# Performance work log

Measured on AMD Instinct MI355X. Metric: run time of the kernel, lower is better.

Reference implementation:

```python
import jax, jax.numpy as jnp
import numpy as np

C = 1024
H = 16
D = C // H  # head_dim = 64
FF = 4 * C


def setup_inputs() -> dict:
    key = jax.random.key(0)
    ks = jax.random.split(key, 10)
    s = lambda fan_in: 1.0 / np.sqrt(fan_in)
    return {
        "x": jax.random.normal(ks[0], (2, 2048, C), dtype=jnp.float32),
        "ln1_g": jnp.ones((C,), jnp.float32),
        "ln1_b": jnp.zeros((C,), jnp.float32),
        "w_qkv": jax.random.normal(ks[1], (C, 3 * C), jnp.float32) * s(C),
        "w_proj": jax.random.normal(ks[2], (C, C), jnp.float32) * s(C),
        "b_proj": jnp.zeros((C,), jnp.float32),
        "ln2_g": jnp.ones((C,), jnp.float32),
        "ln2_b": jnp.zeros((C,), jnp.float32),
        "w_fc1": jax.random.normal(ks[3], (C, FF), jnp.float32) * s(C),
        "b_fc1": jnp.zeros((FF,), jnp.float32),
        "w_fc2": jax.random.normal(ks[4], (FF, C), jnp.float32) * s(FF),
        "b_fc2": jnp.zeros((C,), jnp.float32),
    }


def _layernorm(x, g, b, eps=1e-5):
    mu = jnp.mean(x, axis=-1, keepdims=True)
    var = jnp.var(x, axis=-1, keepdims=True)
    return (x - mu) * jax.lax.rsqrt(var + eps) * g + b


def reference(x, ln1_g, ln1_b, w_qkv, w_proj, b_proj, ln2_g, ln2_b, w_fc1, b_fc1, w_fc2, b_fc2):
    B, N, _ = x.shape
    scale = D ** -0.5
    # --- attention sub-block (pre-LN) ---
    h = _layernorm(x, ln1_g, ln1_b)
    qkv = (h @ w_qkv).reshape(B, N, 3, H, D)
    q, k, v = jnp.moveaxis(qkv, 2, 0)          # each [B, N, H, D]
    attn = jnp.einsum("bnhd,bmhd->bhnm", q, k) * scale  # [B,H,N,N]
    attn = jax.nn.softmax(attn, axis=-1)
    o = jnp.einsum("bhnm,bmhd->bnhd", attn, v).reshape(B, N, C)
    x = x + o @ w_proj + b_proj
    # --- MLP sub-block (pre-LN) ---
    h = _layernorm(x, ln2_g, ln2_b)
    h = jax.nn.gelu(h @ w_fc1 + b_fc1, approximate=False)
    x = x + h @ w_fc2 + b_fc2
    return x
```

## Files before the change

### kernel.cpp

```cpp
#include <hip/hip_runtime.h>
#include <hip/hip_bf16.h>

typedef unsigned short u16;
typedef unsigned int u32;
typedef __attribute__((ext_vector_type(8))) short bf16x8;
typedef __attribute__((ext_vector_type(4))) float f32x4;
typedef __attribute__((ext_vector_type(4))) int   i32x4;
typedef __attribute__((ext_vector_type(4))) float fvec4;
typedef __attribute__((ext_vector_type(4))) unsigned int u32x4;

__device__ inline u16 f2bf(float f) {
    union { float f; unsigned u; } v; v.f = f;
    unsigned r = v.u + 0x7fffu + ((v.u >> 16) & 1u);
    return (u16)(r >> 16);
}

__device__ inline u32 cvtpk(float lo, float hi) {
    u32 r;
    asm("v_cvt_pk_bf16_f32 %0, %1, %2" : "=v"(r) : "v"(lo), "v"(hi));
    return r;
}

__device__ inline f32x4 mfma16(bf16x8 a, bf16x8 b, f32x4 c) {
    return __builtin_amdgcn_mfma_f32_16x16x32_bf16(a, b, c, 0, 0, 0);
}

__device__ inline void gload16(const void* g, void* l) {
    __builtin_amdgcn_global_load_lds(
        (const __attribute__((address_space(1))) unsigned int*)g,
        (__attribute__((address_space(3))) unsigned int*)l, 16, 0, 0);
}

__global__ __launch_bounds__(256)
void transpose_all(const float* __restrict__ w0, u16* __restrict__ o0,
                   const float* __restrict__ w1, u16* __restrict__ o1,
                   const float* __restrict__ w2, u16* __restrict__ o2,
                   const float* __restrict__ w3, u16* __restrict__ o3) {
    __shared__ float tile[32][33];
    int b = blockIdx.x;
    const float* in; u16* out; int K, N, local;
    if (b < 3072)      { in = w0; out = o0; K = 1024; N = 3072; local = b; }
    else if (b < 4096) { in = w1; out = o1; K = 1024; N = 1024; local = b - 3072; }
    else if (b < 8192) { in = w2; out = o2; K = 1024; N = 4096; local = b - 4096; }
    else               { in = w3; out = o3; K = 4096; N = 1024; local = b - 8192; }
    const int nx = N >> 5;
    const int n0 = (local % nx) * 32, k0 = (local / nx) * 32;
    const int x = threadIdx.x & 31, y = threadIdx.x >> 5;
    for (int i = 0; i < 4; ++i)
        tile[y + i * 8][x] = in[(size_t)(k0 + y + i * 8) * N + n0 + x];
    __syncthreads();
    for (int i = 0; i < 4; ++i) {
        int r = y + i * 8;
        out[(size_t)(n0 + r) * K + k0 + x] = f2bf(tile[x][r]);
    }
}

__global__ __launch_bounds__(256)
void vtrans(const u16* __restrict__ qkv, u16* __restrict__ vT) {
    __shared__ u32 tl[64][33];
    const int t0 = blockIdx.x * 64, f0 = blockIdx.y * 64;
    const int a = threadIdx.x & 31, yy = threadIdx.x >> 5;
    for (int i = 0; i < 8; ++i) {
        int t = yy + i * 8;
        tl[t][a] = *(const u32*)(qkv + (size_t)(t0 + t) * 3072 + 2048 + f0 + a * 2);
    }
    __syncthreads();
    for (int i = 0; i < 8; ++i) {
        int f = yy + i * 8;
        u32 lo = tl[2 * a][f >> 1], hi = tl[2 * a + 1][f >> 1];
        u32 r = (f & 1) ? ((lo >> 16) | (hi & 0xffff0000u))
                        : ((lo & 0xffffu) | (hi << 16));
        *(u32*)(vT + (size_t)(f0 + f) * 4096 + t0 + 2 * a) = r;
    }
}

__global__ __launch_bounds__(256)
void ln_kernel(const float* __restrict__ x, const float* __restrict__ g,
               const float* __restrict__ bvec, u16* __restrict__ out) {
    __shared__ float red[2][4];
    const int row = blockIdx.x, tid = threadIdx.x;
    const float* xr = x + (size_t)row * 1024;
    fvec4 v = *(const fvec4*)(xr + tid * 4);
    float s  = v[0] + v[1] + v[2] + v[3];
    float s2 = v[0]*v[0] + v[1]*v[1] + v[2]*v[2] + v[3]*v[3];
    for (int off = 1; off < 64; off <<= 1) {
        s  += __shfl_xor(s,  off);
        s2 += __shfl_xor(s2, off);
    }
    const int w = tid >> 6;
    if ((tid & 63) == 0) { red[0][w] = s; red[1][w] = s2; }
    __syncthreads();
    s  = red[0][0] + red[0][1] + red[0][2] + red[0][3];
    s2 = red[1][0] + red[1][1] + red[1][2] + red[1][3];
    const float mu  = s * (1.0f / 1024.0f);
    const float var = s2 * (1.0f / 1024.0f) - mu * mu;
    const float rstd = rsqrtf(var + 1e-5f);
    fvec4 gv = *(const fvec4*)(g + tid * 4);
    fvec4 bv = *(const fvec4*)(bvec + tid * 4);
    u16 o4[4];
    for (int i = 0; i < 4; ++i)
        o4[i] = f2bf((v[i] - mu) * rstd * gv[i] + bv[i]);
    u32 lo = (u32)o4[0] | ((u32)o4[1] << 16);
    u32 hi = (u32)o4[2] | ((u32)o4[3] << 16);
    u32* dst = (u32*)(out + (size_t)row * 1024 + tid * 4);
    dst[0] = lo; dst[1] = hi;
}

__global__ __launch_bounds__(256)
void reduce4(const float* __restrict__ p1, const float* __restrict__ p2,
             const float* __restrict__ p3, const float* __restrict__ bias,
             const float* __restrict__ res, float* __restrict__ out) {
    const size_t base = (size_t)blockIdx.x * 1024 + threadIdx.x * 4;
    fvec4 a = *(const fvec4*)(out + base);
    fvec4 b = *(const fvec4*)(p1 + base);
    fvec4 c = *(const fvec4*)(p2 + base);
    fvec4 d = *(const fvec4*)(p3 + base);
    fvec4 r = *(const fvec4*)(res + base);
    fvec4 bi = *(const fvec4*)(bias + threadIdx.x * 4);
    fvec4 o;
#pragma unroll
    for (int i = 0; i < 4; ++i) o[i] = ((a[i] + b[i]) + (c[i] + d[i])) + bi[i] + r[i];
    *(fvec4*)(out + base) = o;
}

template <int MODE, int WM, int WN, int MT, int NT, int NYP>
__global__ __launch_bounds__(256)
void gemm64(const u16* __restrict__ A, const u16* __restrict__ Bt,
            const float* __restrict__ bias, const float* __restrict__ res,
            void* __restrict__ out, int M, int N, int K) {
    constexpr int TM = WM * MT * 16;
    constexpr int TN = WN * NT * 16;
    constexpr int AJ = TM / 64;
    constexpr int BJ = TN / 64;
    static_assert(TM == 128, "swizzle assumes 32 M-tiles");
    __shared__ __attribute__((aligned(16))) u16 sA[2 * TM * 32];
    __shared__ __attribute__((aligned(16))) u16 sB[2 * TN * 32];
    const int id = blockIdx.x;
    const int j  = id >> 3;
    const int by = (id & 7) * NYP + (j >> 5);
    const int bx = j & 31;
    const int tid = threadIdx.x;
    const int lane = tid & 63, w = tid >> 6;
    const int wm = w / WN, wn = w % WN;
    const int q = lane >> 4, l16 = lane & 15;

    f32x4 acc[MT][NT];
#pragma unroll
    for (int i = 0; i < MT; ++i)
#pragma unroll
        for (int jj = 0; jj < NT; ++jj) acc[i][jj] = (f32x4)0.0f;

    const int sr = lane >> 2;
    const int kc = (lane & 3) * 8;
    const u16* gA[AJ];
    const u16* gB[BJ];
#pragma unroll
    for (int jj = 0; jj < AJ; ++jj)
        gA[jj] = A + (size_t)(bx * TM + (jj * 4 + w) * 16 + sr) * K + kc;
#pragma unroll
    for (int jj = 0; jj < BJ; ++jj)
        gB[jj] = Bt + (size_t)(by * TN + (jj * 4 + w) * 16 + sr) * K + kc;

    for (int k0 = 0; k0 < K; k0 += 64) {
#pragma unroll
        for (int kt = 0; kt < 2; ++kt) {
#pragma unroll
            for (int jj = 0; jj < AJ; ++jj)
                gload16(gA[jj] + k0 + kt * 32, &sA[kt * TM * 32 + (jj * 4 + w) * 512]);
#pragma unroll
            for (int jj = 0; jj < BJ; ++jj)
                gload16(gB[jj] + k0 + kt * 32, &sB[kt * TN * 32 + (jj * 4 + w) * 512]);
        }
        __syncthreads();
#pragma unroll
        for (int kt = 0; kt < 2; ++kt) {
            bf16x8 af[MT], bf[NT];
#pragma unroll
            for (int mt = 0; mt < MT; ++mt)
                af[mt] = *(const bf16x8*)&sA[kt * TM * 32 +
                         (wm * MT * 16 + mt * 16 + l16) * 32 + q * 8];
#pragma unroll
            for (int nt = 0; nt < NT; ++nt)
                bf[nt] = *(const bf16x8*)&sB[kt * TN * 32 +
                         (wn * NT * 16 + nt * 16 + l16) * 32 + q * 8];
#pragma unroll
            for (int mt = 0; mt < MT; ++mt)
#pragma unroll
                for (int nt = 0; nt < NT; ++nt)
                    acc[mt][nt] = mfma16(af[mt], bf[nt], acc[mt][nt]);
        }
        __syncthreads();
    }

#pragma unroll
    for (int mt = 0; mt < MT; ++mt)
#pragma unroll
        for (int nt = 0; nt < NT; ++nt)
#pragma unroll
            for (int r = 0; r < 4; ++r) {
                const int row = bx * TM + wm * MT * 16 + mt * 16 + q * 4 + r;
                const int col = by * TN + wn * NT * 16 + nt * 16 + l16;
                const size_t idx = (size_t)row * N + col;
                float v = acc[mt][nt][r];
                if (MODE == 0) {
                    ((u16*)out)[idx] = f2bf(v);
                } else if (MODE == 1) {
                    ((float*)out)[idx] = v + bias[col] + res[idx];
                } else {
                    float t = v + bias[col];
                    ((u16*)out)[idx] = f2bf(t * 0.5f * (1.0f + erff(t * 0.70710678118f)));
                }
            }
}

template <int MODE, int SPLIT>
__global__ __launch_bounds__(512)
void gemm256(const u16* __restrict__ A, const u16* __restrict__ Bt,
             const float* __restrict__ bias, const float* __restrict__ res,
             void* __restrict__ out,
             float* __restrict__ q1, float* __restrict__ q2, float* __restrict__ q3,
             int M, int N, int K, int Kc) {
    __shared__ __attribute__((aligned(16))) u16 sA[2][16384];
    __shared__ __attribute__((aligned(16))) u16 sB[2][16384];
    const int tid  = threadIdx.x;
    const int w    = tid >> 6, lane = tid & 63;
    const int wm   = w >> 2,  wn   = w & 3;
    const int q    = lane >> 4, l16 = lane & 15;
    const int w8   = w << 3,  l8   = lane >> 3;
    const int kch  = (lane & 7) ^ l8;

    const int nwg  = gridDim.x;
    const int id   = blockIdx.x;
    const int wgid = (id & 7) * (nwg >> 3) + (id >> 3);
    int bx, by, sp;
    if (SPLIT == 1) { bx = wgid & 15; by = wgid >> 4; sp = 0; }
    else            { bx = wgid & 15; by = (wgid >> 4) & 3; sp = wgid >> 6; }

    const u16* pAs = A  + (size_t)(bx * 256 + w8 + l8) * K + kch * 8 + (size_t)sp * Kc;
    const u16* pBs = Bt + (size_t)(by * 256 + w8 + l8) * K + kch * 8 + (size_t)sp * Kc;

    const int cs0  = ((q ^ (l16 & 7)) << 4);
    const int cs1  = cs0 ^ 64;
    const int aoff = (wm * 128 + l16) * 128;
    const int boff = (wn * 64  + l16) * 128;

    f32x4 acc[8][4];
#pragma unroll
    for (int m = 0; m < 8; ++m)
#pragma unroll
        for (int n = 0; n < 4; ++n) acc[m][n] = (f32x4)0.0f;

#define GISS(P, r0, k0, SH, b_) \
    gload16((P) + (size_t)((r0) * K + (k0)), &SH[b_][((r0) + w8) * 64])

    GISS(pBs, 0, 0, sB, 0);   GISS(pBs, 64, 0, sB, 0);
    GISS(pBs, 128, 0, sB, 0); GISS(pBs, 192, 0, sB, 0);
    GISS(pAs, 0, 0, sA, 0);   GISS(pAs, 64, 0, sA, 0);
    GISS(pAs, 128, 0, sA, 0); GISS(pAs, 192, 0, sA, 0);
    GISS(pBs, 0, 64, sB, 1);  GISS(pBs, 64, 64, sB, 1);
    GISS(pBs, 128, 64, sB, 1);GISS(pBs, 192, 64, sB, 1);
    asm volatile("s_waitcnt vmcnt(4)" ::: "memory");
    __builtin_amdgcn_s_barrier();

    const int NT_ = Kc >> 6;
    for (int t = 0; t < NT_; ++t) {
        const int b  = t & 1;
        const char* bA_ = (const char*)&sA[b][0] + aoff;
        const char* bB_ = (const char*)&sB[b][0] + boff;
        const int kA = (t + 1 < NT_ ? t + 1 : t) << 6;
        const int kB = (t + 2 < NT_ ? t + 2 : t) << 6;

        bf16x8 bfr[4][2];
#pragma unroll
        for (int n = 0; n < 4; ++n) {
            bfr[n][0] = *(const bf16x8*)(bB_ + n * 2048 + cs0);
            bfr[n][1] = *(const bf16x8*)(bB_ + n * 2048 + cs1);
        }
        bf16x8 af[4][2];
#pragma unroll
        for (int m = 0; m < 4; ++m) {
            af[m][0] = *(const bf16x8*)(bA_ + m * 2048 + cs0);
            af[m][1] = *(const bf16x8*)(bA_ + m * 2048 + cs1);
        }
        if (b) { GISS(pAs, 0, kA, sA, 0); GISS(pAs, 64, kA, sA, 0);
                 GISS(pAs, 128, kA, sA, 0); GISS(pAs, 192, kA, sA, 0); }
        else   { GISS(pAs, 0, kA, sA, 1); GISS(pAs, 64, kA, sA, 1);
                 GISS(pAs, 128, kA, sA, 1); GISS(pAs, 192, kA, sA, 1); }
        __builtin_amdgcn_s_setprio(1);
#pragma unroll
        for (int kt = 0; kt < 2; ++kt)
#pragma unroll
            for (int m = 0; m < 4; ++m)
#pragma unroll
                for (int n = 0; n < 4; ++n)
                    acc[m][n] = mfma16(af[m][kt], bfr[n][kt], acc[m][n]);
        __builtin_amdgcn_s_setprio(0);
        __builtin_amdgcn_s_barrier();

        bf16x8 ag[4][2];
#pragma unroll
        for (int m = 0; m < 4; ++m) {
            ag[m][0] = *(const bf16x8*)(bA_ + (4 + m) * 2048 + cs0);
            ag[m][1] = *(const bf16x8*)(bA_ + (4 + m) * 2048 + cs1);
        }
        if (b) { GISS(pBs, 0, kB, sB, 1); GISS(pBs, 64, kB, sB, 1);
                 GISS(pBs, 128, kB, sB, 1); GISS(pBs, 192, kB, sB, 1); }
        else   { GISS(pBs, 0, kB, sB, 0); GISS(pBs, 64, kB, sB, 0);
                 GISS(pBs, 128, kB, sB, 0); GISS(pBs, 192, kB, sB, 0); }
        __builtin_amdgcn_s_setprio(1);
#pragma unroll
        for (int kt = 0; kt < 2; ++kt)
#pragma unroll
            for (int m = 0; m < 4; ++m)
#pragma unroll
                for (int n = 0; n < 4; ++n)
                    acc[4 + m][n] = mfma16(ag[m][kt], bfr[n][kt], acc[4 + m][n]);
        __builtin_amdgcn_s_setprio(0);
        asm volatile("s_waitcnt vmcnt(4)" ::: "memory");
        __builtin_amdgcn_s_barrier();
    }
#undef GISS

    float* po = nullptr;
    if (MODE == 3)
        po = sp == 0 ? (float*)out : sp == 1 ? q1 : sp == 2 ? q2 : q3;

#pragma unroll
    for (int m = 0; m < 8; ++m)
#pragma unroll
        for (int n = 0; n < 4; ++n)
#pragma unroll
            for (int r = 0; r < 4; ++r) {
                const int row = bx * 256 + wm * 128 + m * 16 + q * 4 + r;
                const int col = by * 256 + wn * 64 + n * 16 + l16;
                const size_t idx = (size_t)row * N + col;
                float v = acc[m][n][r];
                if (MODE == 0) {
                    ((u16*)out)[idx] = f2bf(v);
                } else if (MODE == 1) {
                    ((float*)out)[idx] = v + bias[col] + res[idx];
                } else if (MODE == 2) {
                    float t = v + bias[col];
                    ((u16*)out)[idx] = f2bf(t * 0.5f * (1.0f + erff(t * 0.70710678118f)));
                } else {
                    po[idx] = v;
                }
            }
}

__global__ __launch_bounds__(256)
void attention3(const u16* __restrict__ qkv, const u16* __restrict__ vT,
                u16* __restrict__ o) {
    __shared__ __attribute__((aligned(16))) u16 sK[64][72];
    __shared__ __attribute__((aligned(16))) u16 sV[64][72];

    const int tid = threadIdx.x;
    const int lane = tid & 63, w = tid >> 6;
    const int qc = lane >> 4, l16 = lane & 15;
    const int bx = blockIdx.x;
    const int qt = bx & 15, h = (bx >> 4) & 15, b = bx >> 8;
    const int rowbase = qt * 128 + w * 32;

    bf16x8 aQ[2][2];
#pragma unroll
    for (int mtq = 0; mtq < 2; ++mtq)
#pragma unroll
        for (int kd = 0; kd < 2; ++kd)
            aQ[mtq][kd] = *(const bf16x8*)(qkv +
                (size_t)(b * 2048 + rowbase + mtq * 16 + l16) * 3072 +
                h * 64 + kd * 32 + qc * 8);

    f32x4 accO[2][4];
#pragma unroll
    for (int mtq = 0; mtq < 2; ++mtq)
#pragma unroll
        for (int dt = 0; dt < 4; ++dt) accO[mtq][dt] = (f32x4)0.0f;
    f32x4 accS[2];
    accS[0] = (f32x4)0.0f; accS[1] = (f32x4)0.0f;

    bf16x8 vone;
#pragma unroll
    for (int i = 0; i < 8; ++i) vone[i] = (short)0x3F80;

    const int srr = tid >> 3;
    const int sc8 = (tid & 7) * 8;
    const u16* gK = qkv + (size_t)(b * 2048 + srr) * 3072 + 1024 + h * 64 + sc8;
    const u16* gV = vT + (size_t)(h * 64 + srr) * 4096 + b * 2048 + sc8;

    i32x4 cK[2], cV[2];
    cK[0] = *(const i32x4*)gK;
    cK[1] = *(const i32x4*)(gK + (size_t)32 * 3072);
    cV[0] = *(const i32x4*)gV;
    cV[1] = *(const i32x4*)(gV + (size_t)32 * 4096);

    const int sig_base = ((l16 >> 2) << 3) + (l16 & 3);

    for (int kc = 0; kc < 32; ++kc) {
        __syncthreads();
        *(i32x4*)&sK[srr][sc8]      = cK[0];
        *(i32x4*)&sK[srr + 32][sc8] = cK[1];
        *(i32x4*)&sV[srr][sc8]      = cV[0];
        *(i32x4*)&sV[srr + 32][sc8] = cV[1];
        const int kn = (kc + 1 < 32) ? kc + 1 : 31;
        i32x4 nK[2], nV[2];
        nK[0] = *(const i32x4*)(gK + (size_t)kn * 64 * 3072);
        nK[1] = *(const i32x4*)(gK + ((size_t)kn * 64 + 32) * 3072);
        nV[0] = *(const i32x4*)(gV + kn * 64);
        nV[1] = *(const i32x4*)(gV + (size_t)32 * 4096 + kn * 64);
        __syncthreads();

        bf16x8 kf[4][2];
#pragma unroll
        for (int mk = 0; mk < 4; ++mk) {
            const int krow = ((mk & 1) << 5) + ((mk >> 1) << 2) + sig_base;
            kf[mk][0] = *(const bf16x8*)&sK[krow][qc * 8];
            kf[mk][1] = *(const bf16x8*)&sK[krow][32 + qc * 8];
        }

        f32x4 s[2][4];
#pragma unroll
        for (int mtq = 0; mtq < 2; ++mtq)
#pragma unroll
            for (int mk = 0; mk < 4; ++mk) {
                f32x4 z = (f32x4)0.0f;
                z = mfma16(kf[mk][0], aQ[mtq][0], z);
                z = mfma16(kf[mk][1], aQ[mtq][1], z);
                s[mtq][mk] = z;
            }

        bf16x8 pf[2][2];
#pragma unroll
        for (int mtq = 0; mtq < 2; ++mtq) {
#pragma unroll
            for (int mk = 0; mk < 4; ++mk)
#pragma unroll
                for (int r = 0; r < 4; ++r)
                    s[mtq][mk][r] = __expf(s[mtq][mk][r] * 0.125f);
#pragma unroll
            for (int kt = 0; kt < 2; ++kt) {
                u32x4 pw;
                pw[0] = cvtpk(s[mtq][kt][0],     s[mtq][kt][1]);
                pw[1] = cvtpk(s[mtq][kt][2],     s[mtq][kt][3]);
                pw[2] = cvtpk(s[mtq][2 + kt][0], s[mtq][2 + kt][1]);
                pw[3] = cvtpk(s[mtq][2 + kt][2], s[mtq][2 + kt][3]);
                pf[mtq][kt] = *(const bf16x8*)&pw;
            }
        }

#pragma unroll
        for (int kt = 0; kt < 2; ++kt) {
#pragma unroll
            for (int dt = 0; dt < 4; ++dt) {
                bf16x8 vf = *(const bf16x8*)&sV[dt * 16 + l16][kt * 32 + qc * 8];
#pragma unroll
                for (int mtq = 0; mtq < 2; ++mtq)
                    accO[mtq][dt] = mfma16(pf[mtq][kt], vf, accO[mtq][dt]);
            }
#pragma unroll
            for (int mtq = 0; mtq < 2; ++mtq)
                accS[mtq] = mfma16(pf[mtq][kt], vone, accS[mtq]);
        }

        cK[0] = nK[0]; cK[1] = nK[1];
        cV[0] = nV[0]; cV[1] = nV[1];
    }

#pragma unroll
    for (int mtq = 0; mtq < 2; ++mtq)
#pragma unroll
        for (int r = 0; r < 4; ++r) {
            const float inv = 1.0f / accS[mtq][r];
            const size_t tok = (size_t)b * 2048 + rowbase + mtq * 16 + qc * 4 + r;
#pragma unroll
            for (int dt = 0; dt < 4; ++dt)
                o[tok * 1024 + h * 64 + dt * 16 + l16] = f2bf(accO[mtq][dt][r] * inv);
        }
}

extern "C" void kernel_launch(void* const* d_in, const int* in_sizes, int n_in,
                              void* d_out, int out_size, void* d_ws, size_t ws_size,
                              hipStream_t stream) {
    const float* x      = (const float*)d_in[0];
    const float* ln1_g  = (const float*)d_in[1];
    const float* ln1_b  = (const float*)d_in[2];
    const float* w_qkv  = (const float*)d_in[3];
    const float* w_proj = (const float*)d_in[4];
    const float* b_proj = (const float*)d_in[5];
    const float* ln2_g  = (const float*)d_in[6];
    const float* ln2_b  = (const float*)d_in[7];
    const float* w_fc1  = (const float*)d_in[8];
    const float* b_fc1  = (const float*)d_in[9];
    const float* w_fc2  = (const float*)d_in[10];
    const float* b_fc2  = (const float*)d_in[11];
    float* out = (float*)d_out;

    char* ws = (char*)d_ws;
    u16*   wqkvT  = (u16*)(ws + 0);
    u16*   wprojT = (u16*)(ws + 6291456);
    u16*   wfc1T  = (u16*)(ws + 8388608);
    u16*   wfc2T  = (u16*)(ws + 16777216);
    u16*   hA     = (u16*)(ws + 25165824);
    u16*   qkv    = (u16*)(ws + 33554432);
    float* x1     = (float*)(ws + 58720256);
    u16*   gbuf   = (u16*)(ws + 75497472);
    u16*   vT     = (u16*)(ws + 75497472);
    float* p1     = (float*)(ws + 0);
    float* p2     = (float*)(ws + 25165824);
    float* p3     = (float*)(ws + 41943040);

    dim3 blk(256);
    transpose_all<<<12288, blk, 0, stream>>>(w_qkv, wqkvT, w_proj, wprojT,
                                             w_fc1, wfc1T, w_fc2, wfc2T);

    ln_kernel<<<4096, blk, 0, stream>>>(x, ln1_g, ln1_b, hA);
    gemm256<0, 1><<<192, dim3(512), 0, stream>>>(hA, wqkvT, nullptr, nullptr, qkv,
                                                 nullptr, nullptr, nullptr, 4096, 3072, 1024, 1024);
    vtrans<<<dim3(64, 16), blk, 0, stream>>>(qkv, vT);
    attention3<<<512, blk, 0, stream>>>(qkv, vT, hA);
    gemm64<1, 4, 1, 2, 4, 2><<<512, blk, 0, stream>>>(hA, wprojT, b_proj, x, x1, 4096, 1024, 1024);

    u16* h2 = qkv;
    ln_kernel<<<4096, blk, 0, stream>>>(x1, ln2_g, ln2_b, h2);
    gemm256<2, 1><<<256, dim3(512), 0, stream>>>(h2, wfc1T, b_fc1, nullptr, gbuf,
                                                 nullptr, nullptr, nullptr, 4096, 4096, 1024, 1024);
    gemm256<3, 4><<<256, dim3(512), 0, stream>>>(gbuf, wfc2T, nullptr, nullptr, out,
                                                 p1, p2, p3, 4096, 1024, 4096, 1024);
    reduce4<<<4096, blk, 0, stream>>>(p1, p2, p3, b_fc2, x1, out);
}
```

Measured before the change: 348.0 us.

## Double-buffer attention K/V tiles, fold softmax scale into Q, reorder GEMM LDS reads

```diff
diff --git a/kernel.cpp b/kernel.cpp
--- a/kernel.cpp
+++ b/kernel.cpp
@@ -270,22 +270,23 @@
         const int kA = (t + 1 < NT_ ? t + 1 : t) << 6;
         const int kB = (t + 2 < NT_ ? t + 2 : t) << 6;
 
-        bf16x8 bfr[4][2];
-#pragma unroll
-        for (int n = 0; n < 4; ++n) {
-            bfr[n][0] = *(const bf16x8*)(bB_ + n * 2048 + cs0);
-            bfr[n][1] = *(const bf16x8*)(bB_ + n * 2048 + cs1);
-        }
-        bf16x8 af[4][2];
-#pragma unroll
-        for (int m = 0; m < 4; ++m) {
-            af[m][0] = *(const bf16x8*)(bA_ + m * 2048 + cs0);
-            af[m][1] = *(const bf16x8*)(bA_ + m * 2048 + cs1);
-        }
         if (b) { GISS(pAs, 0, kA, sA, 0); GISS(pAs, 64, kA, sA, 0);
                  GISS(pAs, 128, kA, sA, 0); GISS(pAs, 192, kA, sA, 0); }
         else   { GISS(pAs, 0, kA, sA, 1); GISS(pAs, 64, kA, sA, 1);
                  GISS(pAs, 128, kA, sA, 1); GISS(pAs, 192, kA, sA, 1); }
+        bf16x8 bfr[4][2];
+#pragma unroll
+        for (int n = 0; n < 4; ++n) {
+            bfr[n][0] = *(const bf16x8*)(bB_ + n * 2048 + cs0);
+            bfr[n][1] = *(const bf16x8*)(bB_ + n * 2048 + cs1);
+        }
+        bf16x8 af[4][2];
+#pragma unroll
+        for (int m = 0; m < 4; ++m) {
+            af[m][0] = *(const bf16x8*)(bA_ + m * 2048 + cs0);
+            af[m][1] = *(const bf16x8*)(bA_ + m * 2048 + cs1);
+        }
+        __builtin_amdgcn_sched_barrier(0);
         __builtin_amdgcn_s_setprio(1);
 #pragma unroll
         for (int kt = 0; kt < 2; ++kt)
@@ -297,16 +298,17 @@
         __builtin_amdgcn_s_setprio(0);
         __builtin_amdgcn_s_barrier();
 
-        bf16x8 ag[4][2];
-#pragma unroll
-        for (int m = 0; m < 4; ++m) {
-            ag[m][0] = *(const bf16x8*)(bA_ + (4 + m) * 2048 + cs0);
-            ag[m][1] = *(const bf16x8*)(bA_ + (4 + m) * 2048 + cs1);
-        }
         if (b) { GISS(pBs, 0, kB, sB, 1); GISS(pBs, 64, kB, sB, 1);
                  GISS(pBs, 128, kB, sB, 1); GISS(pBs, 192, kB, sB, 1); }
         else   { GISS(pBs, 0, kB, sB, 0); GISS(pBs, 64, kB, sB, 0);
                  GISS(pBs, 128, kB, sB, 0); GISS(pBs, 192, kB, sB, 0); }
+        bf16x8 ag[4][2];
+#pragma unroll
+        for (int m = 0; m < 4; ++m) {
+            ag[m][0] = *(const bf16x8*)(bA_ + (4 + m) * 2048 + cs0);
+            ag[m][1] = *(const bf16x8*)(bA_ + (4 + m) * 2048 + cs1);
+        }
+        __builtin_amdgcn_sched_barrier(0);
         __builtin_amdgcn_s_setprio(1);
 #pragma unroll
         for (int kt = 0; kt < 2; ++kt)
@@ -351,8 +353,8 @@
 __global__ __launch_bounds__(256)
 void attention3(const u16* __restrict__ qkv, const u16* __restrict__ vT,
                 u16* __restrict__ o) {
-    __shared__ __attribute__((aligned(16))) u16 sK[64][72];
-    __shared__ __attribute__((aligned(16))) u16 sV[64][72];
+    __shared__ __attribute__((aligned(16))) u16 sK[2][64][68];
+    __shared__ __attribute__((aligned(16))) u16 sV[2][64][68];
 
     const int tid = threadIdx.x;
     const int lane = tid & 63, w = tid >> 6;
@@ -361,14 +363,26 @@
     const int qt = bx & 15, h = (bx >> 4) & 15, b = bx >> 8;
     const int rowbase = qt * 128 + w * 32;
 
+    const float SC = 0.18033688f;
+
     bf16x8 aQ[2][2];
 #pragma unroll
     for (int mtq = 0; mtq < 2; ++mtq)
 #pragma unroll
-        for (int kd = 0; kd < 2; ++kd)
-            aQ[mtq][kd] = *(const bf16x8*)(qkv +
+        for (int kd = 0; kd < 2; ++kd) {
+            bf16x8 qv = *(const bf16x8*)(qkv +
                 (size_t)(b * 2048 + rowbase + mtq * 16 + l16) * 3072 +
                 h * 64 + kd * 32 + qc * 8);
+            u32x4 pw;
+#pragma unroll
+            for (int i = 0; i < 4; ++i) {
+                union { u32 u; float f; } lo, hi;
+                lo.u = (u32)(u16)(short)qv[2 * i]     << 16;
+                hi.u = (u32)(u16)(short)qv[2 * i + 1] << 16;
+                pw[i] = cvtpk(lo.f * SC, hi.f * SC);
+            }
+            aQ[mtq][kd] = *(const bf16x8*)&pw;
+        }
 
     f32x4 accO[2][4];
 #pragma unroll
@@ -396,11 +410,11 @@
     const int sig_base = ((l16 >> 2) << 3) + (l16 & 3);
 
     for (int kc = 0; kc < 32; ++kc) {
-        __syncthreads();
-        *(i32x4*)&sK[srr][sc8]      = cK[0];
-        *(i32x4*)&sK[srr + 32][sc8] = cK[1];
-        *(i32x4*)&sV[srr][sc8]      = cV[0];
-        *(i32x4*)&sV[srr + 32][sc8] = cV[1];
+        const int p = kc & 1;
+        *(i32x4*)&sK[p][srr][sc8]      = cK[0];
+        *(i32x4*)&sK[p][srr + 32][sc8] = cK[1];
+        *(i32x4*)&sV[p][srr][sc8]      = cV[0];
+        *(i32x4*)&sV[p][srr + 32][sc8] = cV[1];
         const int kn = (kc + 1 < 32) ? kc + 1 : 31;
         i32x4 nK[2], nV[2];
         nK[0] = *(const i32x4*)(gK + (size_t)kn * 64 * 3072);
@@ -413,8 +427,8 @@
 #pragma unroll
         for (int mk = 0; mk < 4; ++mk) {
             const int krow = ((mk & 1) << 5) + ((mk >> 1) << 2) + sig_base;
-            kf[mk][0] = *(const bf16x8*)&sK[krow][qc * 8];
-            kf[mk][1] = *(const bf16x8*)&sK[krow][32 + qc * 8];
+            kf[mk][0] = *(const bf16x8*)&sK[p][krow][qc * 8];
+            kf[mk][1] = *(const bf16x8*)&sK[p][krow][32 + qc * 8];
         }
 
         f32x4 s[2][4];
@@ -435,7 +449,7 @@
             for (int mk = 0; mk < 4; ++mk)
 #pragma unroll
                 for (int r = 0; r < 4; ++r)
-                    s[mtq][mk][r] = __expf(s[mtq][mk][r] * 0.125f);
+                    s[mtq][mk][r] = exp2f(s[mtq][mk][r]);
 #pragma unroll
             for (int kt = 0; kt < 2; ++kt) {
                 u32x4 pw;
@@ -451,7 +465,7 @@
         for (int kt = 0; kt < 2; ++kt) {
 #pragma unroll
             for (int dt = 0; dt < 4; ++dt) {
-                bf16x8 vf = *(const bf16x8*)&sV[dt * 16 + l16][kt * 32 + qc * 8];
+                bf16x8 vf = *(const bf16x8*)&sV[p][dt * 16 + l16][kt * 32 + qc * 8];
 #pragma unroll
                 for (int mtq = 0; mtq < 2; ++mtq)
                     accO[mtq][dt] = mfma16(pf[mtq][kt], vf, accO[mtq][dt]);
```

New measurement: 367.7 us. 1.06x slower.
